# Kernel optimization log

Hardware: AMD Instinct MI355X
Metric: run time of the kernel (lower is better)

Reference implementation:

```python
import jax, jax.numpy as jnp
import numpy as np

ALPHA = 16
M_FACTORS = [8, 16, 8]
N_FACTORS = [8, 16, 8]


def setup_inputs() -> dict:
    key = jax.random.key(0)
    ks = jax.random.split(key, 9)
    B, S, D = 8, 2048, 1024
    r = 8
    x = jax.random.normal(ks[0], (B, S, D), dtype=jnp.float32)
    W = jax.random.normal(ks[1], (D, D), dtype=jnp.float32) * 0.02
    b = jax.random.normal(ks[2], (D,), dtype=jnp.float32) * 0.02
    # m-cores: (r_prev, m_i, r_next), first rank = 1
    core0 = jax.random.normal(ks[3], (1, 8, r), dtype=jnp.float32) * 0.1
    core1 = jax.random.normal(ks[4], (r, 16, r), dtype=jnp.float32) * 0.1
    core2 = jax.random.normal(ks[5], (r, 8, r), dtype=jnp.float32) * 0.1
    # n-cores: (r_prev, n_i, r_next), last rank = 1
    core3 = jax.random.normal(ks[6], (r, 8, r), dtype=jnp.float32) * 0.1
    core4 = jax.random.normal(ks[7], (r, 16, r), dtype=jnp.float32) * 0.1
    core5 = jax.random.normal(ks[8], (r, 8, 1), dtype=jnp.float32) * 0.1
    return {"x": x, "W": W, "b": b, "core0": core0, "core1": core1,
            "core2": core2, "core3": core3, "core4": core4, "core5": core5}


def tensorized_multiplication(x, m_cores, n_cores, m_factors):
    B, S, _ = x.shape
    # [B, 1, S, m_k, ..., m_1] : input dim split into m_factors, reversed
    tt = x.reshape((B, S) + tuple(m_factors[::-1]))[:, None]
    for core in m_cores:
        # contract trailing m-factor and current rank, new rank at axis 1
        tt = jnp.einsum('br...m,rmp->bp...', tt, core)
    for core in n_cores:
        # expand n-factor at the end, carry rank at axis 1
        tt = jnp.einsum('br...,rnp->bp...n', tt, core)
    # tt: [B, 1, S, n_1, ..., n_k] -> [B, S, prod(n_factors)]
    return tt.reshape(B, S, -1)


def reference(x, W, b, core0, core1, core2, core3, core4, core5):
    z = tensorized_multiplication(x, [core0, core1, core2],
                                  [core3, core4, core5], M_FACTORS)
    base = jnp.einsum('bsd,od->bso', x, W) + b  # nn.Linear: x @ W.T + b
    return base + z * ALPHA
```

## Files before the change

### kernel.cpp

```cpp
#include <hip/hip_runtime.h>
#include <hip/hip_bf16.h>


#define D_DIM 1024
#define BS_ROWS 16384
#define ALPHA_F 16.0f
#define BM 128
#define BN 128

using bf16   = __bf16;
using bf16x8 = __attribute__((ext_vector_type(8))) __bf16;
using bf16x4 = __attribute__((ext_vector_type(4))) __bf16;
using f32x4  = __attribute__((ext_vector_type(4))) float;
using f32x16 = __attribute__((ext_vector_type(16))) float;

#define GPTR(p) (const __attribute__((address_space(1))) void*)(p)
#define SPTR(p) (__attribute__((address_space(3))) void*)(p)

__global__ __launch_bounds__(256) void make_mn_kernel(
    const float* __restrict__ c0, const float* __restrict__ c1,
    const float* __restrict__ c2, const float* __restrict__ c3,
    const float* __restrict__ c4, const float* __restrict__ c5,
    float* __restrict__ Mws, float* __restrict__ NTws)
{
    __shared__ float t2[128 * 9];
    __shared__ float vt[128 * 9];
    const int tid = threadIdx.x;

    for (int e = tid; e < 1024; e += 256) {
        int p2 = e & 7, i2i1 = e >> 3;
        int i1 = i2i1 & 7, i2 = i2i1 >> 3;
        float s = 0.f;
        for (int p1 = 0; p1 < 8; ++p1)
            s += c0[i1 * 8 + p1] * c1[p1 * 128 + i2 * 8 + p2];
        t2[i2i1 * 9 + p2] = s;
    }
    __syncthreads();
    for (int e = tid; e < 8192; e += 256) {
        int p3 = e & 7, d = e >> 3;
        int i1 = d & 7, i2 = (d >> 3) & 15, i3 = d >> 7;
        float s = 0.f;
        for (int p2 = 0; p2 < 8; ++p2)
            s += t2[(i2 * 8 + i1) * 9 + p2] * c2[p2 * 64 + i3 * 8 + p3];
        Mws[e] = s;
    }
    for (int e = tid; e < 1024; e += 256) {
        int p4 = e & 7, nn = e >> 3;
        int n2 = nn >> 3, n3 = nn & 7;
        float s = 0.f;
        for (int p5 = 0; p5 < 8; ++p5)
            s += c4[p4 * 128 + n2 * 8 + p5] * c5[p5 * 8 + n3];
        vt[nn * 9 + p4] = s;
    }
    __syncthreads();
    for (int e = tid; e < 8192; e += 256) {
        int r3 = e & 7, o = e >> 3;
        int n1 = o >> 7, nn = o & 127;
        float s = 0.f;
        for (int p4 = 0; p4 < 8; ++p4)
            s += c3[r3 * 64 + n1 * 8 + p4] * vt[nn * 9 + p4];
        NTws[o * 8 + r3] = s;
    }
}

__global__ __launch_bounds__(256) void weff_cast_kernel(
    const float* __restrict__ X, const float* __restrict__ W,
    const float* __restrict__ Mws, const float* __restrict__ NTws,
    bf16* __restrict__ Weff, bf16* __restrict__ Xb)
{
    const int tid = threadIdx.x;
    if (blockIdx.x >= 512) {
        size_t i = ((size_t)(blockIdx.x - 512) * 256 + tid) * 8;
        f32x4 a = *(const f32x4*)&X[i];
        f32x4 b = *(const f32x4*)&X[i + 4];
        bf16x8 v;
        v[0] = (bf16)a[0]; v[1] = (bf16)a[1]; v[2] = (bf16)a[2]; v[3] = (bf16)a[3];
        v[4] = (bf16)b[0]; v[5] = (bf16)b[1]; v[6] = (bf16)b[2]; v[7] = (bf16)b[3];
        *(bf16x8*)&Xb[i] = v;
        return;
    }
    int e  = blockIdx.x * 256 + tid;
    int o  = e >> 7;
    int d0 = (e & 127) * 8;
    f32x4 nt0 = *(const f32x4*)&NTws[o * 8];
    f32x4 nt1 = *(const f32x4*)&NTws[o * 8 + 4];
    f32x4 w0 = *(const f32x4*)&W[(size_t)o * D_DIM + d0];
    f32x4 w1 = *(const f32x4*)&W[(size_t)o * D_DIM + d0 + 4];
    bf16x8 res;
    for (int k = 0; k < 8; ++k) {
        f32x4 m0 = *(const f32x4*)&Mws[(d0 + k) * 8];
        f32x4 m1 = *(const f32x4*)&Mws[(d0 + k) * 8 + 4];
        float acc = m0[0]*nt0[0] + m0[1]*nt0[1] + m0[2]*nt0[2] + m0[3]*nt0[3]
                  + m1[0]*nt1[0] + m1[1]*nt1[1] + m1[2]*nt1[2] + m1[3]*nt1[3];
        float w = (k < 4) ? w0[k] : w1[k - 4];
        res[k] = (bf16)(w + ALPHA_F * acc);
    }
    *(bf16x8*)&Weff[(size_t)o * D_DIM + d0] = res;
}

#define TBM 256
#define TBN 256
#define TBK 32
#define ABYT (TBM * TBK * 2)
#define BBYT (TBN * TBK * 2)
#define BUF2 (ABYT + BBYT)
#define NB2  4
#define NT2  (D_DIM / TBK)

__global__ __launch_bounds__(512, 2) void gemm_pipe2_kernel(
    const bf16* __restrict__ Xb,
    const bf16* __restrict__ Weff,
    const float* __restrict__ bias,
    float* __restrict__ Out)
{
    extern __shared__ __attribute__((aligned(16))) char smem[];

    const int tid  = threadIdx.x;
    const int wave = tid >> 6, lane = tid & 63;

    const int bid   = blockIdx.x;
    const int slot  = (bid & 7) * 32 + (bid >> 3);
    const int mtile = slot >> 2;
    const int ntile = slot & 3;

    const int wr = wave >> 2, wc = wave & 3;
    const int l31 = lane & 31, half = lane >> 5;
    const int swz = (l31 >> 1) & 3;

    const int srow   = wave * 16 + (lane >> 2);
    const int lchunk = (lane & 3) ^ ((lane >> 3) & 3);
    const bf16* asrc = Xb   + (size_t)(mtile * TBM + srow) * D_DIM + lchunk * 8;
    const bf16* bsrc = Weff + (size_t)(ntile * TBN + srow) * D_DIM + lchunk * 8;
    const int woff = wave * 1024;

    auto STAGE = [&](int bo, int t) {
        const bf16* ap = asrc + t * TBK;
        const bf16* bp = bsrc + t * TBK;
        __builtin_amdgcn_global_load_lds(GPTR(ap),
                                         SPTR(smem + bo + woff), 16, 0, 0);
        __builtin_amdgcn_global_load_lds(GPTR(ap + (size_t)128 * D_DIM),
                                         SPTR(smem + bo + 8192 + woff), 16, 0, 0);
        __builtin_amdgcn_global_load_lds(GPTR(bp),
                                         SPTR(smem + bo + ABYT + woff), 16, 0, 0);
        __builtin_amdgcn_global_load_lds(GPTR(bp + (size_t)128 * D_DIM),
                                         SPTR(smem + bo + ABYT + 8192 + woff), 16, 0, 0);
    };

    f32x16 acc[4][2];
#pragma unroll
    for (int i = 0; i < 4; ++i)
#pragma unroll
        for (int j = 0; j < 2; ++j)
#pragma unroll
            for (int r = 0; r < 16; ++r) acc[i][j][r] = 0.f;

    auto COMPUTE = [&](int bo) {
        const char* Ab = smem + bo;
        const char* Bb = smem + bo + ABYT;
#pragma unroll
        for (int kk = 0; kk < 2; ++kk) {
            const int sc16 = (((kk * 2 + half) ^ swz) * 16);
            bf16x8 af[4], bfr[2];
#pragma unroll
            for (int i = 0; i < 4; ++i)
                af[i] = *(const bf16x8*)(Ab + (wr * 128 + i * 32 + l31) * 64 + sc16);
#pragma unroll
            for (int j = 0; j < 2; ++j)
                bfr[j] = *(const bf16x8*)(Bb + (wc * 64 + j * 32 + l31) * 64 + sc16);
            __builtin_amdgcn_s_setprio(1);
#pragma unroll
            for (int i = 0; i < 4; ++i)
#pragma unroll
                for (int j = 0; j < 2; ++j)
                    acc[i][j] = __builtin_amdgcn_mfma_f32_32x32x16_bf16(
                        af[i], bfr[j], acc[i][j], 0, 0, 0);
            __builtin_amdgcn_s_setprio(0);
        }
    };

    STAGE(0, 0);
    STAGE(BUF2, 1);
    STAGE(2 * BUF2, 2);
    asm volatile("s_waitcnt vmcnt(8)" ::: "memory");
    __builtin_amdgcn_s_barrier();
    __builtin_amdgcn_sched_barrier(0);

    int bo = 0;
    for (int t = 0; t < NT2 - 3; ++t) {
        int bs = bo + 3 * BUF2; if (bs >= NB2 * BUF2) bs -= NB2 * BUF2;
        STAGE(bs, t + 3);
        COMPUTE(bo);
        asm volatile("s_waitcnt vmcnt(8) lgkmcnt(0)" ::: "memory");
        __builtin_amdgcn_s_barrier();
        __builtin_amdgcn_sched_barrier(0);
        bo += BUF2; if (bo == NB2 * BUF2) bo = 0;
    }
    COMPUTE(bo);
    asm volatile("s_waitcnt vmcnt(4) lgkmcnt(0)" ::: "memory");
    __builtin_amdgcn_s_barrier();
    __builtin_amdgcn_sched_barrier(0);
    bo += BUF2; if (bo == NB2 * BUF2) bo = 0;
    COMPUTE(bo);
    asm volatile("s_waitcnt vmcnt(0) lgkmcnt(0)" ::: "memory");
    __builtin_amdgcn_s_barrier();
    __builtin_amdgcn_sched_barrier(0);
    bo += BUF2; if (bo == NB2 * BUF2) bo = 0;
    COMPUTE(bo);

    float bj[2];
#pragma unroll
    for (int j = 0; j < 2; ++j)
        bj[j] = bias[ntile * TBN + wc * 64 + j * 32 + l31];
#pragma unroll
    for (int i = 0; i < 4; ++i) {
        int rbase = mtile * TBM + wr * 128 + i * 32 + 4 * half;
#pragma unroll
        for (int j = 0; j < 2; ++j) {
            int col = ntile * TBN + wc * 64 + j * 32 + l31;
#pragma unroll
            for (int r = 0; r < 16; ++r) {
                int row = rbase + (r & 3) + 8 * (r >> 2);
                Out[(size_t)row * D_DIM + col] = acc[i][j][r] + bj[j];
            }
        }
    }
}

__global__ __launch_bounds__(256) void gemm_bb_kernel(
    const bf16* __restrict__ Xb,
    const bf16* __restrict__ Weff,
    const float* __restrict__ bias,
    float* __restrict__ Out)
{
    __shared__ __align__(16) bf16 As[BM][64];
    __shared__ __align__(16) bf16 Bs[BN][64];

    const int tid  = threadIdx.x;
    const int wave = tid >> 6, lane = tid & 63;
    const int mtile = blockIdx.x, ntile = blockIdx.y;
    const int wr = wave >> 1, wc = wave & 1;
    const int l15 = lane & 15, quad = lane >> 4;

    const int srow = wave * 32 + (lane >> 3);
    const int gchunk = (lane & 7) ^ (lane >> 3);
    const bf16* asrc = Xb   + (size_t)(mtile * BM + srow) * D_DIM + gchunk * 8;
    const bf16* bsrc = Weff + (size_t)(ntile * BN + srow) * D_DIM + gchunk * 8;
    char* abase = (char*)&As[0][0] + wave * 4096;
    char* bbase = (char*)&Bs[0][0] + wave * 4096;

    const int rsw = l15 & 7;

    f32x4 acc[4][4];
    for (int i = 0; i < 4; ++i)
        for (int j = 0; j < 4; ++j)
            for (int r = 0; r < 4; ++r) acc[i][j][r] = 0.f;

    for (int kt = 0; kt < D_DIM / 64; ++kt) {
        const int ko = kt * 64;
        for (int j = 0; j < 4; ++j) {
            __builtin_amdgcn_global_load_lds(GPTR(asrc + (size_t)j * 8 * D_DIM + ko),
                                             SPTR(abase + j * 1024), 16, 0, 0);
            __builtin_amdgcn_global_load_lds(GPTR(bsrc + (size_t)j * 8 * D_DIM + ko),
                                             SPTR(bbase + j * 1024), 16, 0, 0);
        }
        __syncthreads();
        for (int kk = 0; kk < 2; ++kk) {
            const int lc = kk * 4 + quad;
            const int sc = (lc ^ rsw) * 8;
            bf16x8 af[4], bfr[4];
            for (int i = 0; i < 4; ++i)
                af[i] = *(const bf16x8*)&As[wr * 64 + i * 16 + l15][sc];
            for (int j = 0; j < 4; ++j)
                bfr[j] = *(const bf16x8*)&Bs[wc * 64 + j * 16 + l15][sc];
            for (int i = 0; i < 4; ++i)
                for (int j = 0; j < 4; ++j)
                    acc[i][j] = __builtin_amdgcn_mfma_f32_16x16x32_bf16(
                        af[i], bfr[j], acc[i][j], 0, 0, 0);
        }
        __syncthreads();
    }

    float bj[4];
    for (int j = 0; j < 4; ++j)
        bj[j] = bias[ntile * BN + wc * 64 + j * 16 + l15];
    for (int i = 0; i < 4; ++i) {
        int row0 = mtile * BM + wr * 64 + i * 16 + quad * 4;
        for (int r = 0; r < 4; ++r) {
            float* orow = Out + (size_t)(row0 + r) * D_DIM + ntile * BN + wc * 64 + l15;
            for (int j = 0; j < 4; ++j)
                orow[j * 16] = acc[i][j][r] + bj[j];
        }
    }
}

__global__ __launch_bounds__(256) void gemm_bias_kernel(
    const float* __restrict__ X,
    const bf16* __restrict__ Weff,
    const float* __restrict__ bias,
    float* __restrict__ Out)
{
    __shared__ __align__(16) bf16 As[BM][32];
    __shared__ __align__(16) bf16 Bs[BN][32];

    const int tid  = threadIdx.x;
    const int wave = tid >> 6, lane = tid & 63;
    const int mtile = blockIdx.x, ntile = blockIdx.y;
    const int wr = wave >> 1, wc = wave & 1;
    const int l15 = lane & 15, quad = lane >> 4;

    const int ar = tid >> 1, ah = tid & 1;
    const float* xsrc = X + (size_t)(mtile * BM + ar) * D_DIM + ah * 16;
    bf16* adst = &As[ar][ah * 16];

    const bf16* bsrc0 = Weff + (size_t)(ntile * BN + wave * 32 + (lane >> 2)) * D_DIM
                        + (lane & 3) * 8;
    const bf16* bsrc1 = bsrc0 + 16 * D_DIM;
    char* bbase = (char*)&Bs[0][0];
    void* bdst0 = bbase + wave * 2048;
    void* bdst1 = bbase + wave * 2048 + 1024;

    f32x4 acc[4][4];
    for (int i = 0; i < 4; ++i)
        for (int j = 0; j < 4; ++j)
            for (int r = 0; r < 4; ++r) acc[i][j][r] = 0.f;

    for (int kt = 0; kt < D_DIM / 32; ++kt) {
        __builtin_amdgcn_global_load_lds(GPTR(bsrc0 + kt * 32), SPTR(bdst0), 16, 0, 0);
        __builtin_amdgcn_global_load_lds(GPTR(bsrc1 + kt * 32), SPTR(bdst1), 16, 0, 0);

        const f32x4* xp = (const f32x4*)(xsrc + kt * 32);
        f32x4 f0 = xp[0], f1 = xp[1], f2 = xp[2], f3 = xp[3];
        bf16x8 p0, p1;
        p0[0] = (bf16)f0[0]; p0[1] = (bf16)f0[1]; p0[2] = (bf16)f0[2]; p0[3] = (bf16)f0[3];
        p0[4] = (bf16)f1[0]; p0[5] = (bf16)f1[1]; p0[6] = (bf16)f1[2]; p0[7] = (bf16)f1[3];
        p1[0] = (bf16)f2[0]; p1[1] = (bf16)f2[1]; p1[2] = (bf16)f2[2]; p1[3] = (bf16)f2[3];
        p1[4] = (bf16)f3[0]; p1[5] = (bf16)f3[1]; p1[6] = (bf16)f3[2]; p1[7] = (bf16)f3[3];
        *(bf16x8*)adst = p0;
        *(bf16x8*)(adst + 8) = p1;

        __syncthreads();

        bf16x8 af[4], bfr[4];
        for (int i = 0; i < 4; ++i)
            af[i] = *(const bf16x8*)&As[wr * 64 + i * 16 + l15][quad * 8];
        for (int j = 0; j < 4; ++j)
            bfr[j] = *(const bf16x8*)&Bs[wc * 64 + j * 16 + l15][quad * 8];
        for (int i = 0; i < 4; ++i)
            for (int j = 0; j < 4; ++j)
                acc[i][j] = __builtin_amdgcn_mfma_f32_16x16x32_bf16(
                    af[i], bfr[j], acc[i][j], 0, 0, 0);

        __syncthreads();
    }

    float bj[4];
    for (int j = 0; j < 4; ++j)
        bj[j] = bias[ntile * BN + wc * 64 + j * 16 + l15];
    for (int i = 0; i < 4; ++i) {
        int row0 = mtile * BM + wr * 64 + i * 16 + quad * 4;
        for (int r = 0; r < 4; ++r) {
            float* orow = Out + (size_t)(row0 + r) * D_DIM + ntile * BN + wc * 64 + l15;
            for (int j = 0; j < 4; ++j)
                orow[j * 16] = acc[i][j][r] + bj[j];
        }
    }
}

__global__ __launch_bounds__(256) void build_weff_fused_kernel(
    const float* __restrict__ W,
    const float* __restrict__ c0, const float* __restrict__ c1,
    const float* __restrict__ c2, const float* __restrict__ c3,
    const float* __restrict__ c4, const float* __restrict__ c5,
    bf16* __restrict__ Weff)
{
    __shared__ float t2[1024];
    __shared__ float Msh[8192];
    const int tid = threadIdx.x;
    const int o = blockIdx.x;

    for (int e = tid; e < 1024; e += 256) {
        int p2 = e & 7, i2i1 = e >> 3;
        int i1 = i2i1 & 7, i2 = i2i1 >> 3;
        float s = 0.f;
        for (int p1 = 0; p1 < 8; ++p1)
            s += c0[i1 * 8 + p1] * c1[p1 * 128 + i2 * 8 + p2];
        t2[e] = s;
    }
    __syncthreads();
    for (int e = tid; e < 8192; e += 256) {
        int p3 = e & 7, d = e >> 3;
        int i1 = d & 7, i2 = (d >> 3) & 15, i3 = d >> 7;
        float s = 0.f;
        for (int p2 = 0; p2 < 8; ++p2)
            s += t2[(i2 * 8 + i1) * 8 + p2] * c2[p2 * 64 + i3 * 8 + p3];
        Msh[e] = s;
    }
    int n1 = o >> 7, nn = o & 127, n2 = nn >> 3, n3 = nn & 7;
    float v[8];
    for (int p4 = 0; p4 < 8; ++p4) {
        float s = 0.f;
        for (int p5 = 0; p5 < 8; ++p5)
            s += c4[p4 * 128 + n2 * 8 + p5] * c5[p5 * 8 + n3];
        v[p4] = s;
    }
    float ncol[8];
    for (int r3 = 0; r3 < 8; ++r3) {
        float s = 0.f;
        for (int p4 = 0; p4 < 8; ++p4)
            s += c3[r3 * 64 + n1 * 8 + p4] * v[p4];
        ncol[r3] = s;
    }
    __syncthreads();

    int d0 = tid * 4;
    f32x4 w = *(const f32x4*)&W[o * D_DIM + d0];
    bf16x4 res;
    for (int k = 0; k < 4; ++k) {
        float acc = 0.f;
        for (int r = 0; r < 8; ++r)
            acc += Msh[(d0 + k) * 8 + r] * ncol[r];
        res[k] = (bf16)(w[k] + ALPHA_F * acc);
    }
    *(bf16x4*)&Weff[o * D_DIM + d0] = res;
}

extern "C" void kernel_launch(void* const* d_in, const int* in_sizes, int n_in,
                              void* d_out, int out_size, void* d_ws, size_t ws_size,
                              hipStream_t stream) {
    const float* x  = (const float*)d_in[0];
    const float* W  = (const float*)d_in[1];
    const float* b  = (const float*)d_in[2];
    const float* c0 = (const float*)d_in[3];
    const float* c1 = (const float*)d_in[4];
    const float* c2 = (const float*)d_in[5];
    const float* c3 = (const float*)d_in[6];
    const float* c4 = (const float*)d_in[7];
    const float* c5 = (const float*)d_in[8];
    float* out = (float*)d_out;

    char* ws = (char*)d_ws;
    bf16*  Weff = (bf16*)ws;
    float* Mws  = (float*)(ws + 2u * 1024u * 1024u);
    float* NTws = Mws + 8192;
    bf16*  Xb   = (bf16*)(ws + 4u * 1024u * 1024u);
    const size_t need = 4u * 1024u * 1024u + (size_t)BS_ROWS * D_DIM * 2u;

    static int smem_ok = -1;
    if (smem_ok < 0) {
        hipError_t e = hipFuncSetAttribute((const void*)gemm_pipe2_kernel,
                                           hipFuncAttributeMaxDynamicSharedMemorySize,
                                           NB2 * BUF2);
        smem_ok = (e == hipSuccess) ? 1 : 0;
    }

    if (ws_size >= need) {
        make_mn_kernel<<<1, 256, 0, stream>>>(c0, c1, c2, c3, c4, c5, Mws, NTws);
        weff_cast_kernel<<<512 + 8192, 256, 0, stream>>>(x, W, Mws, NTws, Weff, Xb);
        if (smem_ok) {
            gemm_pipe2_kernel<<<dim3(256), 512, NB2 * BUF2, stream>>>(Xb, Weff, b, out);
        } else {
            dim3 grid(BS_ROWS / BM, D_DIM / BN);
            gemm_bb_kernel<<<grid, 256, 0, stream>>>(Xb, Weff, b, out);
        }
    } else {
        build_weff_fused_kernel<<<D_DIM, 256, 0, stream>>>(W, c0, c1, c2, c3, c4, c5, Weff);
        dim3 grid(BS_ROWS / BM, D_DIM / BN);
        gemm_bias_kernel<<<grid, 256, 0, stream>>>(x, Weff, b, out);
    }
}
```

Before: 184.6 us.

## Double K tile to 64 with two-buffer pipeline and parallelize TT-core precompute

The GEMM now uses a K tile of 64 with an 8-chunk XOR swizzle and a two-stage double buffer instead of a four-deep ring of K=32 tiles. This halves the number of barrier iterations and gives more MFMAs per sync, at the cost of less prefetch depth and an extra barrier per iteration. The TT-core precompute kernel is split across 64 blocks instead of one, so its serial latency shrinks at the cost of recomputing the small intermediate in every block.

```diff
diff --git a/kernel.cpp b/kernel.cpp
--- a/kernel.cpp
+++ b/kernel.cpp
@@ -23,42 +23,42 @@
     const float* __restrict__ c4, const float* __restrict__ c5,
     float* __restrict__ Mws, float* __restrict__ NTws)
 {
-    __shared__ float t2[128 * 9];
-    __shared__ float vt[128 * 9];
+    __shared__ float sh[128 * 9];
     const int tid = threadIdx.x;
 
-    for (int e = tid; e < 1024; e += 256) {
-        int p2 = e & 7, i2i1 = e >> 3;
-        int i1 = i2i1 & 7, i2 = i2i1 >> 3;
-        float s = 0.f;
-        for (int p1 = 0; p1 < 8; ++p1)
-            s += c0[i1 * 8 + p1] * c1[p1 * 128 + i2 * 8 + p2];
-        t2[i2i1 * 9 + p2] = s;
-    }
-    __syncthreads();
-    for (int e = tid; e < 8192; e += 256) {
+    if (blockIdx.x < 32) {
+        for (int e = tid; e < 1024; e += 256) {
+            int p2 = e & 7, i2i1 = e >> 3;
+            int i1 = i2i1 & 7, i2 = i2i1 >> 3;
+            float s = 0.f;
+            for (int p1 = 0; p1 < 8; ++p1)
+                s += c0[i1 * 8 + p1] * c1[p1 * 128 + i2 * 8 + p2];
+            sh[i2i1 * 9 + p2] = s;
+        }
+        __syncthreads();
+        int e = blockIdx.x * 256 + tid;
         int p3 = e & 7, d = e >> 3;
         int i1 = d & 7, i2 = (d >> 3) & 15, i3 = d >> 7;
         float s = 0.f;
         for (int p2 = 0; p2 < 8; ++p2)
-            s += t2[(i2 * 8 + i1) * 9 + p2] * c2[p2 * 64 + i3 * 8 + p3];
+            s += sh[(i2 * 8 + i1) * 9 + p2] * c2[p2 * 64 + i3 * 8 + p3];
         Mws[e] = s;
-    }
-    for (int e = tid; e < 1024; e += 256) {
-        int p4 = e & 7, nn = e >> 3;
-        int n2 = nn >> 3, n3 = nn & 7;
-        float s = 0.f;
-        for (int p5 = 0; p5 < 8; ++p5)
-            s += c4[p4 * 128 + n2 * 8 + p5] * c5[p5 * 8 + n3];
-        vt[nn * 9 + p4] = s;
-    }
-    __syncthreads();
-    for (int e = tid; e < 8192; e += 256) {
+    } else {
+        for (int e = tid; e < 1024; e += 256) {
+            int p4 = e & 7, nn = e >> 3;
+            int n2 = nn >> 3, n3 = nn & 7;
+            float s = 0.f;
+            for (int p5 = 0; p5 < 8; ++p5)
+                s += c4[p4 * 128 + n2 * 8 + p5] * c5[p5 * 8 + n3];
+            sh[nn * 9 + p4] = s;
+        }
+        __syncthreads();
+        int e = (blockIdx.x - 32) * 256 + tid;
         int r3 = e & 7, o = e >> 3;
         int n1 = o >> 7, nn = o & 127;
         float s = 0.f;
         for (int p4 = 0; p4 < 8; ++p4)
-            s += c3[r3 * 64 + n1 * 8 + p4] * vt[nn * 9 + p4];
+            s += c3[r3 * 64 + n1 * 8 + p4] * sh[nn * 9 + p4];
         NTws[o * 8 + r3] = s;
     }
 }
@@ -100,14 +100,13 @@
 
 #define TBM 256
 #define TBN 256
-#define TBK 32
+#define TBK 64
 #define ABYT (TBM * TBK * 2)
 #define BBYT (TBN * TBK * 2)
-#define BUF2 (ABYT + BBYT)
-#define NB2  4
-#define NT2  (D_DIM / TBK)
-
-__global__ __launch_bounds__(512, 2) void gemm_pipe2_kernel(
+#define BUF4 (ABYT + BBYT)
+#define NT4  (D_DIM / TBK)
+
+__global__ __launch_bounds__(512, 2) void gemm_pipe4_kernel(
     const bf16* __restrict__ Xb,
     const bf16* __restrict__ Weff,
     const float* __restrict__ bias,
@@ -125,25 +124,25 @@
 
     const int wr = wave >> 2, wc = wave & 3;
     const int l31 = lane & 31, half = lane >> 5;
-    const int swz = (l31 >> 1) & 3;
-
-    const int srow   = wave * 16 + (lane >> 2);
-    const int lchunk = (lane & 3) ^ ((lane >> 3) & 3);
-    const bf16* asrc = Xb   + (size_t)(mtile * TBM + srow) * D_DIM + lchunk * 8;
-    const bf16* bsrc = Weff + (size_t)(ntile * TBN + srow) * D_DIM + lchunk * 8;
-    const int woff = wave * 1024;
+    const int rsw = l31 & 7;
+
+    const int srow   = wave * 32 + (lane >> 3);
+    const int gchunk = (lane & 7) ^ (lane >> 3);
+    const bf16* asrc = Xb   + (size_t)(mtile * TBM + srow) * D_DIM + gchunk * 8;
+    const bf16* bsrc = Weff + (size_t)(ntile * TBN + srow) * D_DIM + gchunk * 8;
+    const int woff = wave * 4096;
 
     auto STAGE = [&](int bo, int t) {
         const bf16* ap = asrc + t * TBK;
         const bf16* bp = bsrc + t * TBK;
-        __builtin_amdgcn_global_load_lds(GPTR(ap),
-                                         SPTR(smem + bo + woff), 16, 0, 0);
-        __builtin_amdgcn_global_load_lds(GPTR(ap + (size_t)128 * D_DIM),
-                                         SPTR(smem + bo + 8192 + woff), 16, 0, 0);
-        __builtin_amdgcn_global_load_lds(GPTR(bp),
-                                         SPTR(smem + bo + ABYT + woff), 16, 0, 0);
-        __builtin_amdgcn_global_load_lds(GPTR(bp + (size_t)128 * D_DIM),
-                                         SPTR(smem + bo + ABYT + 8192 + woff), 16, 0, 0);
+#pragma unroll
+        for (int j = 0; j < 4; ++j)
+            __builtin_amdgcn_global_load_lds(GPTR(ap + (size_t)j * 8 * D_DIM),
+                                             SPTR(smem + bo + woff + j * 1024), 16, 0, 0);
+#pragma unroll
+        for (int j = 0; j < 4; ++j)
+            __builtin_amdgcn_global_load_lds(GPTR(bp + (size_t)j * 8 * D_DIM),
+                                             SPTR(smem + bo + ABYT + woff + j * 1024), 16, 0, 0);
     };
 
     f32x16 acc[4][2];
@@ -158,15 +157,15 @@
         const char* Ab = smem + bo;
         const char* Bb = smem + bo + ABYT;
 #pragma unroll
-        for (int kk = 0; kk < 2; ++kk) {
-            const int sc16 = (((kk * 2 + half) ^ swz) * 16);
+        for (int kk = 0; kk < 4; ++kk) {
+            const int sb = (((kk * 2 + half) ^ rsw) * 16);
             bf16x8 af[4], bfr[2];
 #pragma unroll
             for (int i = 0; i < 4; ++i)
-                af[i] = *(const bf16x8*)(Ab + (wr * 128 + i * 32 + l31) * 64 + sc16);
+                af[i] = *(const bf16x8*)(Ab + (wr * 128 + i * 32 + l31) * 128 + sb);
 #pragma unroll
             for (int j = 0; j < 2; ++j)
-                bfr[j] = *(const bf16x8*)(Bb + (wc * 64 + j * 32 + l31) * 64 + sc16);
+                bfr[j] = *(const bf16x8*)(Bb + (wc * 64 + j * 32 + l31) * 128 + sb);
             __builtin_amdgcn_s_setprio(1);
 #pragma unroll
             for (int i = 0; i < 4; ++i)
@@ -179,33 +178,30 @@
     };
 
     STAGE(0, 0);
-    STAGE(BUF2, 1);
-    STAGE(2 * BUF2, 2);
+    STAGE(BUF4, 1);
     asm volatile("s_waitcnt vmcnt(8)" ::: "memory");
     __builtin_amdgcn_s_barrier();
     __builtin_amdgcn_sched_barrier(0);
 
-    int bo = 0;
-    for (int t = 0; t < NT2 - 3; ++t) {
-        int bs = bo + 3 * BUF2; if (bs >= NB2 * BUF2) bs -= NB2 * BUF2;
-        STAGE(bs, t + 3);
+    for (int t = 0; t < NT4 - 2; ++t) {
+        const int bo = (t & 1) * BUF4;
         COMPUTE(bo);
-        asm volatile("s_waitcnt vmcnt(8) lgkmcnt(0)" ::: "memory");
+        asm volatile("s_waitcnt lgkmcnt(0)" ::: "memory");
         __builtin_amdgcn_s_barrier();
         __builtin_amdgcn_sched_barrier(0);
-        bo += BUF2; if (bo == NB2 * BUF2) bo = 0;
-    }
-    COMPUTE(bo);
-    asm volatile("s_waitcnt vmcnt(4) lgkmcnt(0)" ::: "memory");
+        STAGE(bo, t + 2);
+        asm volatile("s_waitcnt vmcnt(8)" ::: "memory");
+        __builtin_amdgcn_s_barrier();
+        __builtin_amdgcn_sched_barrier(0);
+    }
+    COMPUTE(((NT4 - 2) & 1) * BUF4);
+    asm volatile("s_waitcnt lgkmcnt(0)" ::: "memory");
     __builtin_amdgcn_s_barrier();
     __builtin_amdgcn_sched_barrier(0);
-    bo += BUF2; if (bo == NB2 * BUF2) bo = 0;
-    COMPUTE(bo);
-    asm volatile("s_waitcnt vmcnt(0) lgkmcnt(0)" ::: "memory");
+    asm volatile("s_waitcnt vmcnt(0)" ::: "memory");
     __builtin_amdgcn_s_barrier();
     __builtin_amdgcn_sched_barrier(0);
-    bo += BUF2; if (bo == NB2 * BUF2) bo = 0;
-    COMPUTE(bo);
+    COMPUTE(((NT4 - 1) & 1) * BUF4);
 
     float bj[2];
 #pragma unroll
@@ -447,17 +443,17 @@
 
     static int smem_ok = -1;
     if (smem_ok < 0) {
-        hipError_t e = hipFuncSetAttribute((const void*)gemm_pipe2_kernel,
+        hipError_t e = hipFuncSetAttribute((const void*)gemm_pipe4_kernel,
                                            hipFuncAttributeMaxDynamicSharedMemorySize,
-                                           NB2 * BUF2);
+                                           2 * BUF4);
         smem_ok = (e == hipSuccess) ? 1 : 0;
     }
 
     if (ws_size >= need) {
-        make_mn_kernel<<<1, 256, 0, stream>>>(c0, c1, c2, c3, c4, c5, Mws, NTws);
+        make_mn_kernel<<<64, 256, 0, stream>>>(c0, c1, c2, c3, c4, c5, Mws, NTws);
         weff_cast_kernel<<<512 + 8192, 256, 0, stream>>>(x, W, Mws, NTws, Weff, Xb);
         if (smem_ok) {
-            gemm_pipe2_kernel<<<dim3(256), 512, NB2 * BUF2, stream>>>(Xb, Weff, b, out);
+            gemm_pipe4_kernel<<<dim3(256), 512, 2 * BUF4, stream>>>(Xb, Weff, b, out);
         } else {
             dim3 grid(BS_ROWS / BM, D_DIM / BN);
             gemm_bb_kernel<<<grid, 256, 0, stream>>>(Xb, Weff, b, out);
```

Result: faster. 163.9 us (-11.2%).
